# Performance work log

Hardware: AMD Instinct MI355X
Metric: run time of the kernel (lower is better)

The kernel has to match this reference:

```python
import jax, jax.numpy as jnp
import numpy as np

BN_EPS = 1e-5
EPS = 1e-6


def _conv(x, w, pad, dil):
    # NCHW dilated conv, stride 1, no bias (matches nn.Conv2d(bias=False))
    return jax.lax.conv_general_dilated(
        x, w, window_strides=(1, 1), padding=[(pad, pad), (pad, pad)],
        rhs_dilation=(dil, dil), dimension_numbers=('NCHW', 'OIHW', 'NCHW'))


def _bn_relu(x, s, b, m, v):
    # eval-mode batchnorm (running stats) + relu
    inv = (s / jnp.sqrt(v + BN_EPS))[None, :, None, None]
    return jax.nn.relu((x - m[None, :, None, None]) * inv + b[None, :, None, None])


def _l2n(x):
    # l2_norm over channel dim (dim=-2 of [B,C,N]); no eps, as in source
    return x / jnp.linalg.norm(x, axis=1, keepdims=True)


def _forward(x, w1, w2, w3, w4, bn_scale, bn_bias, bn_mean, bn_var,
             wq, bq, wk, bk, wv, bv, gamma):
    B, C, H, W = x.shape
    N = H * W
    # HASP: four dilated-conv branches (dilations 1,6,12,18), concat to 128 ch
    specs = [(w1, 0, 1), (w2, 6, 6), (w3, 12, 12), (w4, 18, 18)]
    branches = [_bn_relu(_conv(x, w, p, d), bn_scale[i], bn_bias[i],
                         bn_mean[i], bn_var[i])
                for i, (w, p, d) in enumerate(specs)]
    x_q = jnp.concatenate(branches, axis=1)  # [B,128,H,W]
    # 1x1 convs as channel GEMMs
    Q = (jnp.einsum('oi,bihw->bohw', wq[:, :, 0, 0], x_q)
         + bq[None, :, None, None]).reshape(B, -1, N)  # [B,16,N]
    K = (jnp.einsum('oi,bihw->bohw', wk[:, :, 0, 0], x)
         + bk[None, :, None, None]).reshape(B, -1, N)  # [B,16,N]
    V = (jnp.einsum('oi,bihw->bohw', wv[:, :, 0, 0], x)
         + bv[None, :, None, None]).reshape(B, -1, N)  # [B,128,N]
    Qn = _l2n(Q).transpose(0, 2, 1)  # [B,N,16]
    Kn = _l2n(K)                     # [B,16,N]
    tailor = 1.0 / (N + jnp.einsum('bnm,bm->bn', Qn, Kn.sum(-1) + EPS))  # [B,N]
    vsum = V.sum(-1)[:, :, None]                      # [B,128,1]
    mat = jnp.einsum('bmn,bcn->bmc', Kn, V)           # [B,16,128]
    msum = vsum + jnp.einsum('bnm,bmc->bcn', Qn, mat)  # [B,128,N]
    out = (msum * tailor[:, None, :]).reshape(B, C, H, W)
    return gamma * out


def setup_inputs() -> dict:
    key = jax.random.key(0)
    ks = jax.random.split(key, 12)
    B, C, H, W = 8, 128, 128, 128
    M = 16  # in_places // scale
    d = {
        'x': jax.random.normal(ks[0], (B, C, H, W), jnp.float32),
        'w1': jax.random.normal(ks[1], (32, 128, 1, 1), jnp.float32) * 0.05,
        'w2': jax.random.normal(ks[2], (32, 128, 3, 3), jnp.float32) * 0.05,
        'w3': jax.random.normal(ks[3], (32, 128, 3, 3), jnp.float32) * 0.05,
        'w4': jax.random.normal(ks[4], (32, 128, 3, 3), jnp.float32) * 0.05,
        'bn_scale': jnp.ones((4, 32), jnp.float32),
        'bn_bias': jnp.zeros((4, 32), jnp.float32),
        'bn_mean': jnp.zeros((4, 32), jnp.float32),
        'bn_var': jnp.ones((4, 32), jnp.float32),
        'wq': jax.random.normal(ks[5], (M, 128, 1, 1), jnp.float32) * 0.05,
        'bq': jax.random.normal(ks[6], (M,), jnp.float32) * 0.05,
        'wk': jax.random.normal(ks[7], (M, 128, 1, 1), jnp.float32) * 0.05,
        'bk': jax.random.normal(ks[8], (M,), jnp.float32) * 0.05,
        'wv': jax.random.normal(ks[9], (C, 128, 1, 1), jnp.float32) * 0.05,
        'bv': jax.random.normal(ks[10], (C,), jnp.float32) * 0.05,
        'gamma': jax.random.uniform(ks[11], (1,), jnp.float32),
    }
    return d


def reference(x, w1, w2, w3, w4, bn_scale, bn_bias, bn_mean, bn_var,
              wq, bq, wk, bk, wv, bv, gamma):
    return _forward(x, w1, w2, w3, w4, bn_scale, bn_bias, bn_mean, bn_var,
                    wq, bq, wk, bk, wv, bv, gamma)
```

## Files before the change

### kernel.cpp

```cpp
#include <hip/hip_runtime.h>
#include <hip/hip_bf16.h>
#include <math.h>

#define NPIX   16384
#define BATCH  8
#define BN_EPS 1e-5f
#define EPS_V  1e-6f

typedef __attribute__((ext_vector_type(8))) short bf16x8;
typedef __attribute__((ext_vector_type(4))) float f32x4;

#define OFF_K     ((size_t)0)
#define OFF_PART2 ((size_t)8192)
#define OFF_W1F   ((size_t)2097152)
#define OFF_WKT   ((size_t)2101248)
#define OFF_WVT   ((size_t)2103296)
#define OFF_BF    ((size_t)2119680)
#define OFF_PART  ((size_t)2119808)
#define OFF_STATS ((size_t)3242112)
#define BASE_END  ((size_t)3259648)
#define OFF_WBT   BASE_END
#define OFF_XT    ((size_t)3314976)
#define OFF_WVB   ((size_t)11703584)
#define NEW_END   ((size_t)11711776)
#define OFF_SQ    OFF_XT
#define OFF_TL    ((size_t)(OFF_XT + 2097152))
#define OFF_W24T  BASE_END

__device__ inline unsigned short f2bf(float f) {
  union { float f; unsigned int u; } v; v.f = f;
  unsigned int r = (v.u + 0x7FFFu + ((v.u >> 16) & 1u)) >> 16;
  return (unsigned short)r;
}

__global__ void prep_common_kernel(const float* __restrict__ w1,
                                   const float* __restrict__ bns, const float* __restrict__ bnb,
                                   const float* __restrict__ bnm, const float* __restrict__ bnv,
                                   const float* __restrict__ wk, const float* __restrict__ wv,
                                   float* __restrict__ w1f, float* __restrict__ wkt,
                                   float* __restrict__ wvt, float* __restrict__ bf) {
  int tid = blockIdx.x * blockDim.x + threadIdx.x;
  int nt  = gridDim.x * blockDim.x;
  for (int i = tid; i < 128; i += nt) {
    float inv = bns[i] * rsqrtf(bnv[i] + BN_EPS);
    bf[i] = bnb[i] - bnm[i] * inv;
  }
  for (int i = tid; i < 4096; i += nt) {
    int c = i >> 5, o = i & 31;
    float inv = bns[o] * rsqrtf(bnv[o] + BN_EPS);
    w1f[i] = w1[o * 128 + c] * inv;
  }
  for (int i = tid; i < 2048; i += nt) {
    int c = i >> 4, m = i & 15;
    wkt[i] = wk[m * 128 + c];
  }
  for (int i = tid; i < 16384; i += nt) {
    int c = i >> 7, o = i & 127;
    wvt[i] = wv[o * 128 + c];
  }
}

__global__ void prep_convb_kernel(const float* __restrict__ w1,
                                  const float* __restrict__ w2, const float* __restrict__ w3,
                                  const float* __restrict__ w4,
                                  const float* __restrict__ bns, const float* __restrict__ bnv,
                                  const float* __restrict__ wk, const float* __restrict__ wv,
                                  unsigned short* __restrict__ wbtr,
                                  unsigned short* __restrict__ wvbr,
                                  unsigned short* __restrict__ wxbr) {
  int tid = blockIdx.x * blockDim.x + threadIdx.x;
  int nt  = gridDim.x * blockDim.x;
  for (int i = tid; i < 16384; i += nt) {
    int e = i & 7, lane = (i >> 3) & 63, f = (i >> 9) & 7, q = i >> 12;
    int oc = f * 16 + (lane & 15);
    int c  = q * 32 + (lane >> 4) * 8 + e;
    wvbr[i] = f2bf(wv[oc * 128 + c]);
  }
  for (int i = tid; i < 6144; i += nt) {
    int e = i & 7, lane = (i >> 3) & 63, ct = i >> 9;
    int tile = ct % 3, q = ct / 3;
    int c = q * 32 + (lane >> 4) * 8 + e;
    float val;
    if (tile < 2) {
      int oc = tile * 16 + (lane & 15);
      val = w1[oc * 128 + c] * (bns[oc] * rsqrtf(bnv[oc] + BN_EPS));
    } else {
      val = wk[(lane & 15) * 128 + c];
    }
    wxbr[i] = f2bf(val);
  }
  for (int i = tid; i < 110592; i += nt) {
    int br = i / 36864;
    int r  = i - br * 36864;
    int tap  = r >> 12;
    int r2   = r & 4095;
    int q    = r2 >> 10;
    int r3   = r2 & 1023;
    int pair = r3 >> 9;
    int r4   = r3 & 511;
    int lane = r4 >> 3, e = r4 & 7;
    int oc = pair * 16 + (lane & 15);
    int c  = q * 32 + (lane >> 4) * 8 + e;
    const float* w = (br == 0) ? w2 : ((br == 1) ? w3 : w4);
    int bo = (br + 1) * 32 + oc;
    float inv = bns[bo] * rsqrtf(bnv[bo] + BN_EPS);
    wbtr[i] = f2bf(w[(oc * 128 + c) * 9 + tap] * inv);
  }
}

__global__ void prep_convf_kernel(const float* __restrict__ w2, const float* __restrict__ w3,
                                  const float* __restrict__ w4,
                                  const float* __restrict__ bns, const float* __restrict__ bnv,
                                  float* __restrict__ w24t) {
  int tid = blockIdx.x * blockDim.x + threadIdx.x;
  int nt  = gridDim.x * blockDim.x;
  for (int i = tid; i < 110592; i += nt) {
    int br  = i / 36864;
    int rem = i - br * 36864;
    int c   = rem / 288;
    int k   = (rem % 288) >> 5;
    int o   = rem & 31;
    const float* w = (br == 0) ? w2 : ((br == 1) ? w3 : w4);
    int bo = (br + 1) * 32 + o;
    float inv = bns[bo] * rsqrtf(bnv[bo] + BN_EPS);
    w24t[i] = w[(o * 128 + c) * 9 + k] * inv;
  }
}

__global__ __launch_bounds__(256) void a0_kernel(const float* __restrict__ x,
                                                 unsigned short* __restrict__ xt) {
  __shared__ unsigned short Ts[64][132];
  int t   = threadIdx.x;
  int b   = blockIdx.y;
  int px0 = blockIdx.x * 64;
  const float* xb = x + (size_t)b * 128 * NPIX;
  int p = t & 63, cq = t >> 6;
#pragma unroll 8
  for (int i = 0; i < 32; ++i) {
    int c = cq * 32 + i;
    Ts[p][c] = f2bf(xb[(size_t)c * NPIX + px0 + p]);
  }
  __syncthreads();
  int pw = t >> 2, cg = t & 3;
  unsigned short* dst = xt + ((size_t)(b * 4 + cg) * 16384 + px0 + pw) * 32;
#pragma unroll
  for (int k = 0; k < 8; ++k) {
    uint2 v = *(const uint2*)(&Ts[pw][cg * 32 + k * 4]);
    *(uint2*)(dst + k * 4) = v;
  }
}

__global__ __launch_bounds__(256) void a1_kernel(const float* __restrict__ x,
                                                 const float* __restrict__ w1f,
                                                 const float* __restrict__ wkt,
                                                 const float* __restrict__ bfp,
                                                 const float* __restrict__ bk,
                                                 float* __restrict__ out,
                                                 float* __restrict__ Kbuf) {
  __shared__ float lw1[128 * 32];
  __shared__ float lwk[128 * 16];
  __shared__ float lbf[32];
  int t = threadIdx.x;
  for (int i = t; i < 4096; i += 256) lw1[i] = w1f[i];
  for (int i = t; i < 2048; i += 256) lwk[i] = wkt[i];
  if (t < 32) lbf[t] = bfp[t];
  __syncthreads();

  int b  = blockIdx.y;
  int px = blockIdx.x * 256 + t;
  const float* xb = x + (size_t)b * 128 * NPIX;

  float acc[48];
#pragma unroll
  for (int i = 0; i < 48; ++i) acc[i] = 0.f;

  for (int c = 0; c < 128; ++c) {
    float xv = xb[(size_t)c * NPIX + px];
    const float4* w1p = (const float4*)(lw1 + c * 32);
#pragma unroll
    for (int j = 0; j < 8; ++j) {
      float4 w = w1p[j];
      acc[j*4+0] = fmaf(w.x, xv, acc[j*4+0]);
      acc[j*4+1] = fmaf(w.y, xv, acc[j*4+1]);
      acc[j*4+2] = fmaf(w.z, xv, acc[j*4+2]);
      acc[j*4+3] = fmaf(w.w, xv, acc[j*4+3]);
    }
    const float4* wkp = (const float4*)(lwk + c * 16);
#pragma unroll
    for (int j = 0; j < 4; ++j) {
      float4 w = wkp[j];
      acc[32+j*4+0] = fmaf(w.x, xv, acc[32+j*4+0]);
      acc[32+j*4+1] = fmaf(w.y, xv, acc[32+j*4+1]);
      acc[32+j*4+2] = fmaf(w.z, xv, acc[32+j*4+2]);
      acc[32+j*4+3] = fmaf(w.w, xv, acc[32+j*4+3]);
    }
  }
#pragma unroll
  for (int o = 0; o < 32; ++o)
    out[((size_t)(b * 128 + o)) * NPIX + px] = fmaxf(acc[o] + lbf[o], 0.f);
#pragma unroll
  for (int m = 0; m < 16; ++m)
    Kbuf[((size_t)(b * 16 + m)) * NPIX + px] = acc[32 + m] + bk[m];
}

__global__ __launch_bounds__(256) void a2m_kernel(const unsigned short* __restrict__ xt,
                                                  const unsigned short* __restrict__ wbtr,
                                                  const float* __restrict__ bfp,
                                                  float* __restrict__ out) {
  __shared__ uint4 sxv[3073];
  unsigned short* sx = (unsigned short*)sxv;
  int t    = threadIdx.x;
  int wave = t >> 6, lane = t & 63;
  int l15  = lane & 15, cg = lane >> 4;
  int idx  = blockIdx.x;
  int b    = idx & 7;
  int rest = idx >> 3;
  int h2   = rest & 63;
  int br   = rest >> 6;
  int d    = 6 * (br + 1);
  int h0   = h2 * 2;
  int j    = wave >> 1;
  int p0   = (wave & 1) * 64;

  if (t == 0) sxv[3072] = make_uint4(0u, 0u, 0u, 0u);

  const unsigned short* wb = wbtr + (size_t)br * 36864;

  f32x4 acc[2][4];
#pragma unroll
  for (int i = 0; i < 2; ++i)
#pragma unroll
    for (int n = 0; n < 4; ++n) acc[i][n] = (f32x4){0.f, 0.f, 0.f, 0.f};

  int pxb[3], xorv[3];
#pragma unroll
  for (int kw = 0; kw < 3; ++kw) {
    pxb[kw]  = p0 + l15 + (kw - 1) * d;
    xorv[kw] = (cg ^ ((pxb[kw] >> 1) & 3)) << 4;
  }

  for (int q = 0; q < 4; ++q) {
    __syncthreads();
    const unsigned short* slab = xt + (size_t)(b * 4 + q) * 524288;
    uint4 stv[12];
#pragma unroll
    for (int k = 0; k < 12; ++k) {
      int slot = k >> 1;
      int srow = h0 + (slot & 1) + ((slot >> 1) - 1) * d;
      int su   = ((k & 1) << 8) + t;
      if ((unsigned)srow < 128u)
        stv[k] = *(const uint4*)(slab + (size_t)srow * 4096 + su * 8);
      else
        stv[k] = make_uint4(0u, 0u, 0u, 0u);
    }
#pragma unroll
    for (int k = 0; k < 12; ++k) {
      int slot = k >> 1;
      int su   = ((k & 1) << 8) + t;
      int px   = su >> 2, cgs = su & 3;
      int phys = slot * 4096 + px * 32 + ((cgs ^ ((px >> 1) & 3)) << 3);
      *(uint4*)(sx + phys) = stv[k];
    }
    __syncthreads();
#pragma unroll
    for (int kh = 0; kh < 3; ++kh) {
      int slot  = kh * 2 + j;
      int sbase = slot * 8192;
      bf16x8 a[3][2];
#pragma unroll
      for (int kw = 0; kw < 3; ++kw) {
        int tap = kh * 3 + kw;
        const unsigned short* wt = wb + ((((size_t)tap * 4 + q) * 2) << 9);
        a[kw][0] = *(const bf16x8*)(wt + lane * 8);
        a[kw][1] = *(const bf16x8*)(wt + 512 + lane * 8);
      }
#pragma unroll
      for (int kw = 0; kw < 3; ++kw) {
        int base = sbase + pxb[kw] * 64 + xorv[kw];
#pragma unroll
        for (int nf = 0; nf < 4; ++nf) {
          int px   = pxb[kw] + nf * 16;
          int addr = ((unsigned)px < 128u) ? (base + nf * 1024) : 49152;
          bf16x8 bv = *(const bf16x8*)((const char*)sx + addr);
          acc[0][nf] = __builtin_amdgcn_mfma_f32_16x16x32_bf16(a[kw][0], bv, acc[0][nf], 0, 0, 0);
          acc[1][nf] = __builtin_amdgcn_mfma_f32_16x16x32_bf16(a[kw][1], bv, acc[1][nf], 0, 0, 0);
        }
      }
    }
  }

  int ocb = (br + 1) * 32;
  int pxw = (h0 + j) * 128 + p0;
#pragma unroll
  for (int mf = 0; mf < 2; ++mf) {
#pragma unroll
    for (int r = 0; r < 4; ++r) {
      int oc = mf * 16 + cg * 4 + r;
      float bias = bfp[ocb + oc];
      float* op = out + ((size_t)(b * 128 + ocb + oc)) * NPIX + pxw + l15;
#pragma unroll
      for (int nf = 0; nf < 4; ++nf)
        op[nf * 16] = fmaxf(acc[mf][nf][r] + bias, 0.f);
    }
  }
}

__global__ __launch_bounds__(256) void a2f_kernel(const float* __restrict__ x,
                                                  const float* __restrict__ w24t,
                                                  const float* __restrict__ bfp,
                                                  float* __restrict__ out) {
  int t  = threadIdx.x;
  int og = t & 3;
  int pg = (t >> 2) & 15;
  int r  = t >> 6;
  int br = blockIdx.z;
  int b  = blockIdx.y;
  int h  = blockIdx.x * 4 + r;
  int d  = 6 * (br + 1);

  const float* wt = w24t + (size_t)br * 36864;
  const float* bf = bfp + (br + 1) * 32;
  const float* xb = x + (size_t)b * 128 * NPIX;
  int w0 = pg << 3;

  float acc[8][8];
#pragma unroll
  for (int p = 0; p < 8; ++p)
#pragma unroll
    for (int o = 0; o < 8; ++o) acc[p][o] = 0.f;

  for (int c = 0; c < 128; ++c) {
    const float* xc = xb + (size_t)c * NPIX;
    const float* wc = wt + c * 288;
#pragma unroll
    for (int kh = 0; kh < 3; ++kh) {
      int row = h + (kh - 1) * d;
      if ((unsigned)row >= 128u) continue;
      const float* xr = xc + row * 128;
#pragma unroll
      for (int kw = 0; kw < 3; ++kw) {
        int wb = w0 + (kw - 1) * d;
        float xv[8];
        if (wb >= 0 && wb <= 120) {
          const float2* p2 = (const float2*)(xr + wb);
#pragma unroll
          for (int jj = 0; jj < 4; ++jj) {
            float2 v = p2[jj];
            xv[2*jj] = v.x; xv[2*jj+1] = v.y;
          }
        } else {
#pragma unroll
          for (int jj = 0; jj < 8; ++jj) {
            int ww = wb + jj;
            xv[jj] = ((unsigned)ww < 128u) ? xr[ww] : 0.f;
          }
        }
        const float4* wp = (const float4*)(wc + (kh * 3 + kw) * 32 + og * 8);
        float4 wa = wp[0], wbv = wp[1];
        float wr[8] = {wa.x, wa.y, wa.z, wa.w, wbv.x, wbv.y, wbv.z, wbv.w};
#pragma unroll
        for (int p = 0; p < 8; ++p)
#pragma unroll
          for (int o = 0; o < 8; ++o)
            acc[p][o] = fmaf(xv[p], wr[o], acc[p][o]);
      }
    }
  }

  int chbase = (br + 1) * 32 + og * 8;
  int n = h * 128 + w0;
#pragma unroll
  for (int o = 0; o < 8; ++o) {
    float bias = bf[og * 8 + o];
    float* op = out + ((size_t)(b * 128 + chbase + o)) * NPIX + n;
    float4 v0 = make_float4(fmaxf(acc[0][o] + bias, 0.f), fmaxf(acc[1][o] + bias, 0.f),
                            fmaxf(acc[2][o] + bias, 0.f), fmaxf(acc[3][o] + bias, 0.f));
    float4 v1 = make_float4(fmaxf(acc[4][o] + bias, 0.f), fmaxf(acc[5][o] + bias, 0.f),
                            fmaxf(acc[6][o] + bias, 0.f), fmaxf(acc[7][o] + bias, 0.f));
    ((float4*)op)[0] = v0;
    ((float4*)op)[1] = v1;
  }
}

__global__ __launch_bounds__(256) void cm_kernel(const unsigned short* __restrict__ xt,
                                                 const unsigned short* __restrict__ wvbr,
                                                 const unsigned short* __restrict__ wxbr,
                                                 const float* __restrict__ bv,
                                                 const float* __restrict__ bfp,
                                                 const float* __restrict__ bk,
                                                 float* __restrict__ out,
                                                 float* __restrict__ part1,
                                                 float* __restrict__ part2) {
  __shared__ __align__(16) unsigned short Vl[128 * 136];
  __shared__ __align__(16) unsigned short knl[16 * 136];
  int t    = threadIdx.x;
  int idx  = blockIdx.x;
  int b    = idx & 7;
  int blk  = idx >> 3;
  int wave = t >> 6, lane = t & 63;
  int l15  = lane & 15, cg = lane >> 4;
  int ocb  = wave * 32;
  int pbase = blk << 7;

  float bvr[2][4];
#pragma unroll
  for (int mf = 0; mf < 2; ++mf)
#pragma unroll
    for (int r = 0; r < 4; ++r) bvr[mf][r] = bv[ocb + mf * 16 + cg * 4 + r];

  float xb4[4];
#pragma unroll
  for (int r = 0; r < 4; ++r) xb4[r] = 0.f;
  if (wave == 0) {
#pragma unroll
    for (int r = 0; r < 4; ++r) xb4[r] = bfp[cg * 4 + r];
  } else if (wave == 1) {
#pragma unroll
    for (int r = 0; r < 4; ++r) xb4[r] = bfp[16 + cg * 4 + r];
  } else if (wave == 2) {
#pragma unroll
    for (int r = 0; r < 4; ++r) xb4[r] = bk[cg * 4 + r];
  }
  int xwave = (wave < 3) ? wave : 0;

  float kr[4] = {0.f, 0.f, 0.f, 0.f};
  float sv[2][4];
#pragma unroll
  for (int mf = 0; mf < 2; ++mf)
#pragma unroll
    for (int r = 0; r < 4; ++r) sv[mf][r] = 0.f;
  f32x4 am[2];
  am[0] = (f32x4){0.f,0.f,0.f,0.f};
  am[1] = (f32x4){0.f,0.f,0.f,0.f};

#pragma unroll
  for (int hf = 0; hf < 2; ++hf) {
    f32x4 vacc[2][4];
    f32x4 xacc[4];
#pragma unroll
    for (int i = 0; i < 2; ++i)
#pragma unroll
      for (int n = 0; n < 4; ++n) vacc[i][n] = (f32x4){0.f,0.f,0.f,0.f};
#pragma unroll
    for (int n = 0; n < 4; ++n) xacc[n] = (f32x4){0.f,0.f,0.f,0.f};

#pragma unroll
    for (int cc = 0; cc < 4; ++cc) {
      const unsigned short* xq = xt + ((size_t)(b * 4 + cc) * 16384 + pbase) * 32;
      bf16x8 a0 = *(const bf16x8*)(wvbr + ((cc * 8 + wave * 2 + 0) << 9) + lane * 8);
      bf16x8 a1 = *(const bf16x8*)(wvbr + ((cc * 8 + wave * 2 + 1) << 9) + lane * 8);
      bf16x8 ax = *(const bf16x8*)(wxbr + ((cc * 3 + xwave) << 9) + lane * 8);
#pragma unroll
      for (int nf = 0; nf < 4; ++nf) {
        int nfg = hf * 4 + nf;
        bf16x8 bx = *(const bf16x8*)(xq + (size_t)(nfg * 16 + l15) * 32 + cg * 8);
        vacc[0][nf] = __builtin_amdgcn_mfma_f32_16x16x32_bf16(a0, bx, vacc[0][nf], 0, 0, 0);
        vacc[1][nf] = __builtin_amdgcn_mfma_f32_16x16x32_bf16(a1, bx, vacc[1][nf], 0, 0, 0);
        if (wave < 3)
          xacc[nf] = __builtin_amdgcn_mfma_f32_16x16x32_bf16(ax, bx, xacc[nf], 0, 0, 0);
      }
    }

#pragma unroll
    for (int mf = 0; mf < 2; ++mf) {
#pragma unroll
      for (int r = 0; r < 4; ++r) {
        float s = 0.f;
#pragma unroll
        for (int nf = 0; nf < 4; ++nf) s += vacc[mf][nf][r];
        sv[mf][r] += s;
        int c = ocb + mf * 16 + cg * 4 + r;
#pragma unroll
        for (int nf = 0; nf < 4; ++nf)
          Vl[c * 136 + (hf * 4 + nf) * 16 + l15] = f2bf(vacc[mf][nf][r] + bvr[mf][r]);
      }
    }

    if (wave < 2) {
#pragma unroll
      for (int r = 0; r < 4; ++r) {
        int oc = wave * 16 + cg * 4 + r;
        float* op = out + ((size_t)(b * 128 + oc)) * NPIX + pbase + l15;
#pragma unroll
        for (int nf = 0; nf < 4; ++nf)
          op[(hf * 4 + nf) * 16] = fmaxf(xacc[nf][r] + xb4[r], 0.f);
      }
    } else if (wave == 2) {
#pragma unroll
      for (int nf = 0; nf < 4; ++nf) {
        int nfg = hf * 4 + nf;
        float kq[4]; float s2 = 0.f;
#pragma unroll
        for (int r = 0; r < 4; ++r) {
          kq[r] = xacc[nf][r] + xb4[r];
          s2 = fmaf(kq[r], kq[r], s2);
        }
        s2 += __shfl_xor(s2, 16);
        s2 += __shfl_xor(s2, 32);
        float inv = rsqrtf(s2);
#pragma unroll
        for (int r = 0; r < 4; ++r) {
          float kn = kq[r] * inv;
          knl[(cg * 4 + r) * 136 + nfg * 16 + l15] = f2bf(kn);
          kr[r] += kn;
        }
      }
    }
  }
  __syncthreads();

#pragma unroll
  for (int ks = 0; ks < 4; ++ks) {
    bf16x8 af = *(const bf16x8*)(knl + l15 * 136 + ks * 32 + cg * 8);
    bf16x8 b0 = *(const bf16x8*)(Vl + (size_t)(ocb + l15) * 136 + ks * 32 + cg * 8);
    bf16x8 b1 = *(const bf16x8*)(Vl + (size_t)(ocb + 16 + l15) * 136 + ks * 32 + cg * 8);
    am[0] = __builtin_amdgcn_mfma_f32_16x16x32_bf16(af, b0, am[0], 0, 0, 0);
    am[1] = __builtin_amdgcn_mfma_f32_16x16x32_bf16(af, b1, am[1], 0, 0, 0);
  }

  float* pp = (blk < 64) ? (part1 + ((size_t)b * 64 + blk) * 2192)
                         : (part2 + ((size_t)b * 64 + (blk - 64)) * 2192);
#pragma unroll
  for (int nf2 = 0; nf2 < 2; ++nf2)
#pragma unroll
    for (int r = 0; r < 4; ++r)
      pp[(cg * 4 + r) * 128 + ocb + nf2 * 16 + l15] = am[nf2][r];
#pragma unroll
  for (int off = 1; off < 16; off <<= 1) {
#pragma unroll
    for (int mf = 0; mf < 2; ++mf)
#pragma unroll
      for (int r = 0; r < 4; ++r)
        sv[mf][r] += __shfl_xor(sv[mf][r], off);
  }
  if (l15 == 0) {
#pragma unroll
    for (int mf = 0; mf < 2; ++mf)
#pragma unroll
      for (int r = 0; r < 4; ++r) {
        int c = ocb + mf * 16 + cg * 4 + r;
        pp[2048 + c] = sv[mf][r] + 128.f * bv[c];
      }
  }
  if (wave == 2) {
#pragma unroll
    for (int off = 1; off < 16; off <<= 1) {
#pragma unroll
      for (int r = 0; r < 4; ++r)
        kr[r] += __shfl_xor(kr[r], off);
    }
    if (l15 == 0) {
#pragma unroll
      for (int r = 0; r < 4; ++r)
        pp[2048 + 128 + cg * 4 + r] = kr[r];
    }
  }
}

__global__ __launch_bounds__(256) void cf_kernel(const float* __restrict__ x,
                                                 const float* __restrict__ bv,
                                                 const float* __restrict__ Kbuf,
                                                 const float* __restrict__ wvt,
                                                 float* __restrict__ part) {
  __shared__ float Vl[128 * 129];
  __shared__ float knl[16 * 132];
  int t   = threadIdx.x;
  int b   = blockIdx.y;
  int blk = blockIdx.x;
  const float* Kb = Kbuf + (size_t)b * 16 * NPIX;
  const float* xb = x + (size_t)b * 128 * NPIX;

  int m_own = t & 15;
  int c0    = (t >> 4) << 3;
  int pxg   = t & 15;

  float bvr[8];
#pragma unroll
  for (int jj = 0; jj < 8; ++jj) bvr[jj] = bv[c0 + jj];

  float macc[8] = {0,0,0,0,0,0,0,0};
  float vs[8]   = {0,0,0,0,0,0,0,0};
  float ksum[16];
#pragma unroll
  for (int m = 0; m < 16; ++m) ksum[m] = 0.f;

  for (int tile = blk; tile < 128; tile += 64) {
    __syncthreads();
    int pbase = tile << 7;

    if (t < 128) {
      float kv[16]; float ss = 0.f;
#pragma unroll
      for (int m = 0; m < 16; ++m) {
        kv[m] = Kb[(size_t)m * NPIX + pbase + t];
        ss = fmaf(kv[m], kv[m], ss);
      }
      float inv = rsqrtf(ss);
#pragma unroll
      for (int m = 0; m < 16; ++m) {
        float kn = kv[m] * inv;
        knl[m * 132 + t] = kn;
        ksum[m] += kn;
      }
    }

    float v[8][8];
#pragma unroll
    for (int i = 0; i < 8; ++i)
#pragma unroll
      for (int jj = 0; jj < 8; ++jj) v[i][jj] = 0.f;
    int px0 = pbase + (pxg << 3);
    for (int k = 0; k < 128; ++k) {
      const float4* xp = (const float4*)(xb + (size_t)k * NPIX + px0);
      float4 xa = xp[0], xc4 = xp[1];
      const float4* wp = (const float4*)(wvt + k * 128 + c0);
      float4 wa = wp[0], wc4 = wp[1];
      float xv[8] = {xa.x, xa.y, xa.z, xa.w, xc4.x, xc4.y, xc4.z, xc4.w};
      float wr[8] = {wa.x, wa.y, wa.z, wa.w, wc4.x, wc4.y, wc4.z, wc4.w};
#pragma unroll
      for (int i = 0; i < 8; ++i)
#pragma unroll
        for (int jj = 0; jj < 8; ++jj)
          v[i][jj] = fmaf(wr[i], xv[jj], v[i][jj]);
    }
#pragma unroll
    for (int i = 0; i < 8; ++i)
#pragma unroll
      for (int jj = 0; jj < 8; ++jj)
        Vl[(c0 + i) * 129 + (pxg << 3) + jj] = v[i][jj] + bvr[i];
    __syncthreads();

    for (int px = 0; px < 128; ++px) {
      float knv = knl[m_own * 132 + px];
      float vv[8];
#pragma unroll
      for (int jj = 0; jj < 8; ++jj) vv[jj] = Vl[(c0 + jj) * 129 + px];
#pragma unroll
      for (int jj = 0; jj < 8; ++jj) macc[jj] = fmaf(knv, vv[jj], macc[jj]);
      if (m_own == 0) {
#pragma unroll
        for (int jj = 0; jj < 8; ++jj) vs[jj] += vv[jj];
      }
    }
  }

  int blkid = b * 64 + blk;
  float* pp = part + (size_t)blkid * 2192;
#pragma unroll
  for (int jj = 0; jj < 8; ++jj) pp[m_own * 128 + c0 + jj] = macc[jj];
  if (m_own == 0) {
#pragma unroll
    for (int jj = 0; jj < 8; ++jj) pp[2048 + c0 + jj] = vs[jj];
  }
  __syncthreads();
  if (t < 128) {
#pragma unroll
    for (int m = 0; m < 16; ++m) knl[m * 132 + t] = ksum[m];
  }
  __syncthreads();
  if (t < 16) {
    float s = 0.f;
    for (int i = 0; i < 128; ++i) s += knl[t * 132 + i];
    pp[2048 + 128 + t] = s;
  }
}

__global__ void reduce_kernel(const float* __restrict__ part, float* __restrict__ stats) {
  int b = blockIdx.y, t = threadIdx.x;
  int e = blockIdx.x * 256 + t;
  if (e >= 2192) return;
  const float* pp = part + (size_t)b * 64 * 2192;
  float s = 0.f;
  for (int g = 0; g < 64; ++g) s += pp[(size_t)g * 2192 + e];
  stats[(size_t)b * 2192 + e] = s;
}

__global__ void reduce2_kernel(const float* __restrict__ part1,
                               const float* __restrict__ part2,
                               float* __restrict__ stats) {
  int b = blockIdx.y, t = threadIdx.x;
  int e = blockIdx.x * 256 + t;
  if (e >= 2192) return;
  const float* p1 = part1 + (size_t)b * 64 * 2192;
  const float* p2 = part2 + (size_t)b * 64 * 2192;
  float s = 0.f;
  for (int g = 0; g < 64; ++g) s += p1[(size_t)g * 2192 + e];
  for (int g = 0; g < 64; ++g) s += p2[(size_t)g * 2192 + e];
  stats[(size_t)b * 2192 + e] = s;
}

__global__ __launch_bounds__(256) void d1_kernel(const float* __restrict__ stats,
                                                 const float* __restrict__ wq,
                                                 const float* __restrict__ bq,
                                                 const float* __restrict__ gamma,
                                                 const float* __restrict__ out,
                                                 float* __restrict__ sq,
                                                 float* __restrict__ tlb) {
  __shared__ float wql[128 * 16];
  __shared__ float ksl[16];
  int t = threadIdx.x;
  int b = blockIdx.y;
  const float* st = stats + (size_t)b * 2192;
  for (int i = t; i < 2048; i += 256) {
    int m = i >> 7, c = i & 127;
    wql[c * 16 + m] = wq[m * 128 + c];
  }
  if (t < 16) ksl[t] = st[2048 + 128 + t] + EPS_V;
  __syncthreads();

  int px = blockIdx.x * 256 + t;
  const float* ob = out + (size_t)b * 128 * NPIX;

  float q[16];
#pragma unroll
  for (int m = 0; m < 16; ++m) q[m] = bq[m];
  for (int c = 0; c < 128; ++c) {
    float xv = ob[(size_t)c * NPIX + px];
    const float4* wp = (const float4*)(wql + c * 16);
#pragma unroll
    for (int jj = 0; jj < 4; ++jj) {
      float4 w = wp[jj];
      q[jj*4+0] = fmaf(w.x, xv, q[jj*4+0]);
      q[jj*4+1] = fmaf(w.y, xv, q[jj*4+1]);
      q[jj*4+2] = fmaf(w.z, xv, q[jj*4+2]);
      q[jj*4+3] = fmaf(w.w, xv, q[jj*4+3]);
    }
  }
  float ss = 0.f;
#pragma unroll
  for (int m = 0; m < 16; ++m) ss = fmaf(q[m], q[m], ss);
  float inv = rsqrtf(ss);
#pragma unroll
  for (int m = 0; m < 16; ++m) q[m] *= inv;
  float den = (float)NPIX;
#pragma unroll
  for (int m = 0; m < 16; ++m) den = fmaf(q[m], ksl[m], den);
  float tl = gamma[0] / den;

  tlb[(size_t)b * NPIX + px] = tl;
#pragma unroll
  for (int m = 0; m < 16; ++m)
    sq[((size_t)(b * 16 + m)) * NPIX + px] = tl * q[m];
}

__global__ __launch_bounds__(256) void d2_kernel(const float* __restrict__ stats,
                                                 const float* __restrict__ sq,
                                                 const float* __restrict__ tlb,
                                                 float* __restrict__ out) {
  __shared__ float matl[128 * 16];
  __shared__ float vsl[128];
  int t = threadIdx.x;
  int b = blockIdx.y;
  const float* st = stats + (size_t)b * 2192;
  for (int i = t; i < 2048; i += 256) {
    int m = i >> 7, c = i & 127;
    matl[c * 16 + m] = st[i];
  }
  if (t < 128) vsl[t] = st[2048 + t];
  __syncthreads();

  int px = blockIdx.x * 256 + t;
  float* ob = out + (size_t)b * 128 * NPIX;

  float tlv = tlb[(size_t)b * NPIX + px];
  float sv[16];
#pragma unroll
  for (int m = 0; m < 16; ++m)
    sv[m] = sq[((size_t)(b * 16 + m)) * NPIX + px];

  for (int c = 0; c < 128; ++c) {
    float s = vsl[c] * tlv;
    const float4* mp = (const float4*)(matl + c * 16);
#pragma unroll
    for (int jj = 0; jj < 4; ++jj) {
      float4 w = mp[jj];
      s = fmaf(w.x, sv[jj*4+0], s);
      s = fmaf(w.y, sv[jj*4+1], s);
      s = fmaf(w.z, sv[jj*4+2], s);
      s = fmaf(w.w, sv[jj*4+3], s);
    }
    ob[(size_t)c * NPIX + px] = s;
  }
}

__global__ __launch_bounds__(256) void df_kernel(const float* __restrict__ stats,
                                                 const float* __restrict__ wq,
                                                 const float* __restrict__ bq,
                                                 const float* __restrict__ gamma,
                                                 float* __restrict__ out) {
  __shared__ float matl[128 * 16];
  __shared__ float wql[128 * 16];
  __shared__ float vsl[128];
  __shared__ float ksl[16];
  int t = threadIdx.x;
  int b = blockIdx.y;
  const float* st = stats + (size_t)b * 2192;
  for (int i = t; i < 2048; i += 256) {
    int m = i >> 7, c = i & 127;
    matl[c * 16 + m] = st[i];
    wql[c * 16 + m]  = wq[m * 128 + c];
  }
  if (t < 128) vsl[t] = st[2048 + t];
  if (t < 16)  ksl[t] = st[2048 + 128 + t] + EPS_V;
  __syncthreads();

  int px = blockIdx.x * 256 + t;
  float* ob = out + (size_t)b * 128 * NPIX;

  float q[16];
#pragma unroll
  for (int m = 0; m < 16; ++m) q[m] = bq[m];
  for (int c = 0; c < 128; ++c) {
    float xv = ob[(size_t)c * NPIX + px];
    const float4* wp = (const float4*)(wql + c * 16);
#pragma unroll
    for (int jj = 0; jj < 4; ++jj) {
      float4 w = wp[jj];
      q[jj*4+0] = fmaf(w.x, xv, q[jj*4+0]);
      q[jj*4+1] = fmaf(w.y, xv, q[jj*4+1]);
      q[jj*4+2] = fmaf(w.z, xv, q[jj*4+2]);
      q[jj*4+3] = fmaf(w.w, xv, q[jj*4+3]);
    }
  }
  float ss = 0.f;
#pragma unroll
  for (int m = 0; m < 16; ++m) ss = fmaf(q[m], q[m], ss);
  float inv = rsqrtf(ss);
#pragma unroll
  for (int m = 0; m < 16; ++m) q[m] *= inv;
  float den = (float)NPIX;
#pragma unroll
  for (int m = 0; m < 16; ++m) den = fmaf(q[m], ksl[m], den);
  float tl = gamma[0] / den;

  for (int c = 0; c < 128; ++c) {
    float s = vsl[c];
    const float4* mp = (const float4*)(matl + c * 16);
#pragma unroll
    for (int jj = 0; jj < 4; ++jj) {
      float4 w = mp[jj];
      s = fmaf(w.x, q[jj*4+0], s);
      s = fmaf(w.y, q[jj*4+1], s);
      s = fmaf(w.z, q[jj*4+2], s);
      s = fmaf(w.w, q[jj*4+3], s);
    }
    ob[(size_t)c * NPIX + px] = tl * s;
  }
}

extern "C" void kernel_launch(void* const* d_in, const int* in_sizes, int n_in,
                              void* d_out, int out_size, void* d_ws, size_t ws_size,
                              hipStream_t stream) {
  (void)in_sizes; (void)n_in; (void)out_size;
  const float* x   = (const float*)d_in[0];
  const float* w1  = (const float*)d_in[1];
  const float* w2  = (const float*)d_in[2];
  const float* w3  = (const float*)d_in[3];
  const float* w4  = (const float*)d_in[4];
  const float* bns = (const float*)d_in[5];
  const float* bnb = (const float*)d_in[6];
  const float* bnm = (const float*)d_in[7];
  const float* bnv = (const float*)d_in[8];
  const float* wq  = (const float*)d_in[9];
  const float* bq  = (const float*)d_in[10];
  const float* wk  = (const float*)d_in[11];
  const float* bk  = (const float*)d_in[12];
  const float* wv  = (const float*)d_in[13];
  const float* bv  = (const float*)d_in[14];
  const float* gm  = (const float*)d_in[15];
  float* ws  = (float*)d_ws;
  float* out = (float*)d_out;

  float* Kbuf = ws + OFF_K;
  float* w1f  = ws + OFF_W1F;
  float* wkt  = ws + OFF_WKT;
  float* wvt  = ws + OFF_WVT;
  float* bfp  = ws + OFF_BF;
  float* part = ws + OFF_PART;
  float* stat = ws + OFF_STATS;

  prep_common_kernel<<<64, 256, 0, stream>>>(w1, bns, bnb, bnm, bnv, wk, wv,
                                             w1f, wkt, wvt, bfp);

  bool use_mfma = ws_size >= NEW_END * sizeof(float);
  if (use_mfma) {
    unsigned short* wbtr = (unsigned short*)(ws + OFF_WBT);
    unsigned short* xt   = (unsigned short*)(ws + OFF_XT);
    unsigned short* wvbr = (unsigned short*)(ws + OFF_WVB);
    unsigned short* wxbr = (unsigned short*)(ws + OFF_K);
    float* part2 = ws + OFF_PART2;
    float* sq  = ws + OFF_SQ;
    float* tlb = ws + OFF_TL;
    prep_convb_kernel<<<64, 256, 0, stream>>>(w1, w2, w3, w4, bns, bnv, wk, wv,
                                              wbtr, wvbr, wxbr);
    a0_kernel<<<dim3(256, 8), 256, 0, stream>>>(x, xt);
    a2m_kernel<<<dim3(1536), 256, 0, stream>>>(xt, wbtr, bfp, out);
    cm_kernel<<<dim3(1024), 256, 0, stream>>>(xt, wvbr, wxbr, bv, bfp, bk, out, part, part2);
    reduce2_kernel<<<dim3(9, 8), 256, 0, stream>>>(part, part2, stat);
    d1_kernel<<<dim3(64, 8), 256, 0, stream>>>(stat, wq, bq, gm, out, sq, tlb);
    d2_kernel<<<dim3(64, 8), 256, 0, stream>>>(stat, sq, tlb, out);
  } else {
    float* w24t = ws + OFF_W24T;
    prep_convf_kernel<<<64, 256, 0, stream>>>(w2, w3, w4, bns, bnv, w24t);
    a1_kernel<<<dim3(64, 8), 256, 0, stream>>>(x, w1f, wkt, bfp, bk, out, Kbuf);
    a2f_kernel<<<dim3(32, 8, 3), 256, 0, stream>>>(x, w24t, bfp, out);
    cf_kernel<<<dim3(64, 8), 256, 0, stream>>>(x, bv, Kbuf, wvt, part);
    reduce_kernel<<<dim3(9, 8), 256, 0, stream>>>(part, stat);
    df_kernel<<<dim3(64, 8), 256, 0, stream>>>(stat, wq, bq, gm, out);
  }
}
```

Measured before the change: 148.0 us.

## Pipeline dilated conv staging with direct global-to-LDS loads and triple buffering

```diff
diff --git a/kernel.cpp b/kernel.cpp
--- a/kernel.cpp
+++ b/kernel.cpp
@@ -9,6 +9,8 @@
 
 typedef __attribute__((ext_vector_type(8))) short bf16x8;
 typedef __attribute__((ext_vector_type(4))) float f32x4;
+typedef const __attribute__((address_space(1))) unsigned int* gas_ptr;
+typedef __attribute__((address_space(3))) unsigned int* las_ptr;
 
 #define OFF_K     ((size_t)0)
 #define OFF_PART2 ((size_t)8192)
@@ -22,7 +24,8 @@
 #define OFF_WBT   BASE_END
 #define OFF_XT    ((size_t)3314976)
 #define OFF_WVB   ((size_t)11703584)
-#define NEW_END   ((size_t)11711776)
+#define OFF_ZROW  ((size_t)11711776)
+#define NEW_END   ((size_t)11713824)
 #define OFF_SQ    OFF_XT
 #define OFF_TL    ((size_t)(OFF_XT + 2097152))
 #define OFF_W24T  BASE_END
@@ -67,9 +70,11 @@
                                   const float* __restrict__ wk, const float* __restrict__ wv,
                                   unsigned short* __restrict__ wbtr,
                                   unsigned short* __restrict__ wvbr,
-                                  unsigned short* __restrict__ wxbr) {
+                                  unsigned short* __restrict__ wxbr,
+                                  unsigned short* __restrict__ zrow) {
   int tid = blockIdx.x * blockDim.x + threadIdx.x;
   int nt  = gridDim.x * blockDim.x;
+  for (int i = tid; i < 4096; i += nt) zrow[i] = 0;
   for (int i = tid; i < 16384; i += nt) {
     int e = i & 7, lane = (i >> 3) & 63, f = (i >> 9) & 7, q = i >> 12;
     int oc = f * 16 + (lane & 15);
@@ -143,10 +148,12 @@
   __syncthreads();
   int pw = t >> 2, cg = t & 3;
   unsigned short* dst = xt + ((size_t)(b * 4 + cg) * 16384 + px0 + pw) * 32;
+  int sw = (pw >> 1) & 3;
 #pragma unroll
   for (int k = 0; k < 8; ++k) {
     uint2 v = *(const uint2*)(&Ts[pw][cg * 32 + k * 4]);
-    *(uint2*)(dst + k * 4) = v;
+    int cgs = (k >> 1) ^ sw;
+    *(uint2*)(dst + cgs * 8 + (k & 1) * 4) = v;
   }
 }
 
@@ -204,11 +211,11 @@
 }
 
 __global__ __launch_bounds__(256) void a2m_kernel(const unsigned short* __restrict__ xt,
+                                                  const unsigned short* __restrict__ zrow,
                                                   const unsigned short* __restrict__ wbtr,
                                                   const float* __restrict__ bfp,
                                                   float* __restrict__ out) {
-  __shared__ uint4 sxv[3073];
-  unsigned short* sx = (unsigned short*)sxv;
+  __shared__ unsigned short sx[3 * 8192 + 8];
   int t    = threadIdx.x;
   int wave = t >> 6, lane = t & 63;
   int l15  = lane & 15, cg = lane >> 4;
@@ -220,11 +227,13 @@
   int d    = 6 * (br + 1);
   int h0   = h2 * 2;
   int j    = wave >> 1;
-  int p0   = (wave & 1) * 64;
-
-  if (t == 0) sxv[3072] = make_uint4(0u, 0u, 0u, 0u);
-
-  const unsigned short* wb = wbtr + (size_t)br * 36864;
+  int whalf = wave & 1;
+  int p0   = whalf * 64;
+
+  if (t == 0) *(uint4*)(sx + 24576) = make_uint4(0u, 0u, 0u, 0u);
+
+  const unsigned short* wb    = wbtr + (size_t)br * 36864;
+  const unsigned short* slabs = xt + (size_t)b * 4 * 524288;
 
   f32x4 acc[2][4];
 #pragma unroll
@@ -239,54 +248,51 @@
     xorv[kw] = (cg ^ ((pxb[kw] >> 1) & 3)) << 4;
   }
 
-  for (int q = 0; q < 4; ++q) {
+  auto STAGE = [&](int s) {
+    int q = s / 3, kh = s % 3;
+    int srow = h0 + j + (kh - 1) * d;
+    const unsigned short* rowsrc =
+        ((unsigned)srow < 128u) ? (slabs + (size_t)q * 524288 + (size_t)srow * 4096)
+                                : zrow;
+    const unsigned short* gsrc = rowsrc + whalf * 2048 + lane * 8;
+    unsigned short* lbase = sx + (s % 3) * 8192 + j * 4096 + whalf * 2048;
+#pragma unroll
+    for (int k = 0; k < 4; ++k)
+      __builtin_amdgcn_global_load_lds((gas_ptr)(const void*)(gsrc + k * 512),
+                                       (las_ptr)(void*)(lbase + k * 512), 16, 0, 0);
+  };
+
+  auto COMPUTE = [&](int s) {
+    int q = s / 3, kh = s % 3;
+    int bb = (s % 3) * 16384 + j * 8192;
+    bf16x8 a[3][2];
+#pragma unroll
+    for (int kw = 0; kw < 3; ++kw) {
+      int tap = kh * 3 + kw;
+      const unsigned short* wt = wb + ((((size_t)tap * 4 + q) * 2) << 9);
+      a[kw][0] = *(const bf16x8*)(wt + lane * 8);
+      a[kw][1] = *(const bf16x8*)(wt + 512 + lane * 8);
+    }
+#pragma unroll
+    for (int kw = 0; kw < 3; ++kw) {
+      int base = bb + pxb[kw] * 64 + xorv[kw];
+#pragma unroll
+      for (int nf = 0; nf < 4; ++nf) {
+        int px   = pxb[kw] + nf * 16;
+        int addr = ((unsigned)px < 128u) ? (base + nf * 1024) : 49152;
+        bf16x8 bv = *(const bf16x8*)((const char*)sx + addr);
+        acc[0][nf] = __builtin_amdgcn_mfma_f32_16x16x32_bf16(a[kw][0], bv, acc[0][nf], 0, 0, 0);
+        acc[1][nf] = __builtin_amdgcn_mfma_f32_16x16x32_bf16(a[kw][1], bv, acc[1][nf], 0, 0, 0);
+      }
+    }
+  };
+
+  STAGE(0);
+  __syncthreads();
+  for (int s = 0; s < 12; ++s) {
+    if (s < 11) STAGE(s + 1);
+    COMPUTE(s);
     __syncthreads();
-    const unsigned short* slab = xt + (size_t)(b * 4 + q) * 524288;
-    uint4 stv[12];
-#pragma unroll
-    for (int k = 0; k < 12; ++k) {
-      int slot = k >> 1;
-      int srow = h0 + (slot & 1) + ((slot >> 1) - 1) * d;
-      int su   = ((k & 1) << 8) + t;
-      if ((unsigned)srow < 128u)
-        stv[k] = *(const uint4*)(slab + (size_t)srow * 4096 + su * 8);
-      else
-        stv[k] = make_uint4(0u, 0u, 0u, 0u);
-    }
-#pragma unroll
-    for (int k = 0; k < 12; ++k) {
-      int slot = k >> 1;
-      int su   = ((k & 1) << 8) + t;
-      int px   = su >> 2, cgs = su & 3;
-      int phys = slot * 4096 + px * 32 + ((cgs ^ ((px >> 1) & 3)) << 3);
-      *(uint4*)(sx + phys) = stv[k];
-    }
-    __syncthreads();
-#pragma unroll
-    for (int kh = 0; kh < 3; ++kh) {
-      int slot  = kh * 2 + j;
-      int sbase = slot * 8192;
-      bf16x8 a[3][2];
-#pragma unroll
-      for (int kw = 0; kw < 3; ++kw) {
-        int tap = kh * 3 + kw;
-        const unsigned short* wt = wb + ((((size_t)tap * 4 + q) * 2) << 9);
-        a[kw][0] = *(const bf16x8*)(wt + lane * 8);
-        a[kw][1] = *(const bf16x8*)(wt + 512 + lane * 8);
-      }
-#pragma unroll
-      for (int kw = 0; kw < 3; ++kw) {
-        int base = sbase + pxb[kw] * 64 + xorv[kw];
-#pragma unroll
-        for (int nf = 0; nf < 4; ++nf) {
-          int px   = pxb[kw] + nf * 16;
-          int addr = ((unsigned)px < 128u) ? (base + nf * 1024) : 49152;
-          bf16x8 bv = *(const bf16x8*)((const char*)sx + addr);
-          acc[0][nf] = __builtin_amdgcn_mfma_f32_16x16x32_bf16(a[kw][0], bv, acc[0][nf], 0, 0, 0);
-          acc[1][nf] = __builtin_amdgcn_mfma_f32_16x16x32_bf16(a[kw][1], bv, acc[1][nf], 0, 0, 0);
-        }
-      }
-    }
   }
 
   int ocb = (br + 1) * 32;
@@ -401,6 +407,7 @@
   int l15  = lane & 15, cg = lane >> 4;
   int ocb  = wave * 32;
   int pbase = blk << 7;
+  int cgsw = (cg ^ ((l15 >> 1) & 3)) << 3;
 
   float bvr[2][4];
 #pragma unroll
@@ -453,7 +460,7 @@
 #pragma unroll
       for (int nf = 0; nf < 4; ++nf) {
         int nfg = hf * 4 + nf;
-        bf16x8 bx = *(const bf16x8*)(xq + (size_t)(nfg * 16 + l15) * 32 + cg * 8);
+        bf16x8 bx = *(const bf16x8*)(xq + (size_t)(nfg * 16 + l15) * 32 + cgsw);
         vacc[0][nf] = __builtin_amdgcn_mfma_f32_16x16x32_bf16(a0, bx, vacc[0][nf], 0, 0, 0);
         vacc[1][nf] = __builtin_amdgcn_mfma_f32_16x16x32_bf16(a1, bx, vacc[1][nf], 0, 0, 0);
         if (wave < 3)
@@ -887,14 +894,15 @@
     unsigned short* wbtr = (unsigned short*)(ws + OFF_WBT);
     unsigned short* xt   = (unsigned short*)(ws + OFF_XT);
     unsigned short* wvbr = (unsigned short*)(ws + OFF_WVB);
+    unsigned short* zrow = (unsigned short*)(ws + OFF_ZROW);
     unsigned short* wxbr = (unsigned short*)(ws + OFF_K);
     float* part2 = ws + OFF_PART2;
     float* sq  = ws + OFF_SQ;
     float* tlb = ws + OFF_TL;
     prep_convb_kernel<<<64, 256, 0, stream>>>(w1, w2, w3, w4, bns, bnv, wk, wv,
-                                              wbtr, wvbr, wxbr);
+                                              wbtr, wvbr, wxbr, zrow);
     a0_kernel<<<dim3(256, 8), 256, 0, stream>>>(x, xt);
-    a2m_kernel<<<dim3(1536), 256, 0, stream>>>(xt, wbtr, bfp, out);
+    a2m_kernel<<<dim3(1536), 256, 0, stream>>>(xt, zrow, wbtr, bfp, out);
     cm_kernel<<<dim3(1024), 256, 0, stream>>>(xt, wvbr, wxbr, bv, bfp, bk, out, part, part2);
     reduce2_kernel<<<dim3(9, 8), 256, 0, stream>>>(part, part2, stat);
     d1_kernel<<<dim3(64, 8), 256, 0, stream>>>(stat, wq, bq, gm, out, sq, tlb);
```

After: 146.2 us. Within noise of the previous version (-1.2%).
